# Optimization experiments

Measured on AMD Instinct MI355X. Metric: run time of the kernel, lower is better.

## Reference

```python
import jax, jax.numpy as jnp
import numpy as np

BERT_VOCAB_SIZE = 28996
INPUT_SIZE = 768
HIDDEN = 512
BI_H = 2 * HIDDEN


def _gru_cell(x, h, wih, whh, bih, bhh):
    # PyTorch GRUCell math. x: [I], h: [H]; wih: [3H, I], whh: [3H, H]
    H = h.shape[-1]
    gx = wih @ x + bih            # [3H]
    gh = whh @ h + bhh            # [3H]
    r = jax.nn.sigmoid(gx[:H] + gh[:H])
    z = jax.nn.sigmoid(gx[H:2 * H] + gh[H:2 * H])
    n = jnp.tanh(gx[2 * H:] + r * gh[2 * H:])
    return (1.0 - z) * n + z * h


def _run_gru(xs, h0, wih, whh, bih, bhh):
    def step(h, x):
        hn = _gru_cell(x, h, wih, whh, bih, bhh)
        return hn, hn
    _, hs = jax.lax.scan(step, h0, xs)
    return hs  # [L, H]


def setup_inputs() -> dict:
    key = jax.random.key(0)
    ks = jax.random.split(key, 16)
    s = 0.02
    inp = {
        'input_context': jax.random.normal(ks[0], (512, INPUT_SIZE), jnp.float32),
        'output_context': jax.random.normal(ks[1], (1024, INPUT_SIZE), jnp.float32),
        # forward encoder GRUCell
        'fw_wih': jax.random.normal(ks[2], (3 * HIDDEN, INPUT_SIZE), jnp.float32) * s,
        'fw_whh': jax.random.normal(ks[3], (3 * HIDDEN, HIDDEN), jnp.float32) * s,
        'fw_bih': jnp.zeros((3 * HIDDEN,), jnp.float32),
        'fw_bhh': jnp.zeros((3 * HIDDEN,), jnp.float32),
        # backward encoder GRUCell
        'bw_wih': jax.random.normal(ks[4], (3 * HIDDEN, INPUT_SIZE), jnp.float32) * s,
        'bw_whh': jax.random.normal(ks[5], (3 * HIDDEN, HIDDEN), jnp.float32) * s,
        'bw_bih': jnp.zeros((3 * HIDDEN,), jnp.float32),
        'bw_bhh': jnp.zeros((3 * HIDDEN,), jnp.float32),
        # decoder GRUCell (hidden = 2H)
        'dec_wih': jax.random.normal(ks[6], (3 * BI_H, INPUT_SIZE), jnp.float32) * s,
        'dec_whh': jax.random.normal(ks[7], (3 * BI_H, BI_H), jnp.float32) * s,
        'dec_bih': jnp.zeros((3 * BI_H,), jnp.float32),
        'dec_bhh': jnp.zeros((3 * BI_H,), jnp.float32),
        # vocab projection
        'W_pred': jax.random.normal(ks[8], (BI_H, BERT_VOCAB_SIZE), jnp.float32) * s,
    }
    return inp


def reference(input_context, output_context,
              fw_wih, fw_whh, fw_bih, fw_bhh,
              bw_wih, bw_whh, bw_bih, bw_bhh,
              dec_wih, dec_whh, dec_bih, dec_bhh,
              W_pred):
    h0 = jnp.zeros((HIDDEN,), input_context.dtype)
    # bidirectional encoder
    fwd_hs = _run_gru(input_context, h0, fw_wih, fw_whh, fw_bih, fw_bhh)        # [L, H]
    bwd_hs = _run_gru(input_context[::-1], h0, bw_wih, bw_whh, bw_bih, bw_bhh)[::-1]
    # column L-1 of cat((fwd, bwd), dim=0) -> [fwd_hs[-1]; bwd_hs[-1]]
    h_dec0 = jnp.concatenate([fwd_hs[-1], bwd_hs[-1]], axis=0)                   # [2H]
    # decoder inputs: step 0 uses output_context[0], step i>0 uses output_context[i-1]
    dec_in = jnp.concatenate([output_context[:1], output_context[:-1]], axis=0)  # [Lo, I]
    dec_hs = _run_gru(dec_in, h_dec0, dec_wih, dec_whh, dec_bih, dec_bhh)        # [Lo, 2H]
    preds = dec_hs @ W_pred                                                      # [Lo, V]
    return preds
```

## Files before the change

### kernel.cpp

```cpp
#include <hip/hip_runtime.h>
#include <math.h>


typedef unsigned long long u64;
typedef unsigned short ushort_t;
typedef __attribute__((ext_vector_type(8))) short short8;
typedef __attribute__((ext_vector_type(4))) float f32x4;

#define NV 28996
#define NRWG 64
#define NWORK 192
#define TRT 7264
#define VOCT 1816

__device__ __forceinline__ float sigmoidf_(float x) {
  return 1.0f / (1.0f + __expf(-x));
}
__device__ __forceinline__ float tanhf_(float x) {
  const float xx = fminf(fmaxf(x, -15.0f), 15.0f);
  const float e = __expf(2.0f * xx);
  return (e - 1.0f) / (e + 1.0f);
}
__device__ __forceinline__ ushort_t f2bf(float f) {
  union { float f; unsigned u; } c; c.f = f;
  unsigned u = c.u;
  u += 0x7fffu + ((u >> 16) & 1u);
  return (ushort_t)(u >> 16);
}

__device__ __forceinline__ u64 pack_ht(float h, unsigned tag) {
  union { float f; unsigned u; } c; c.f = h;
  return ((u64)tag << 32) | (u64)c.u;
}
__device__ __forceinline__ float pk_h(u64 v) {
  union { unsigned u; float f; } c; c.u = (unsigned)v; return c.f;
}
__device__ __forceinline__ void astore(u64* p, u64 v) {
  __hip_atomic_store(p, v, __ATOMIC_RELAXED, __HIP_MEMORY_SCOPE_AGENT);
}
__device__ __forceinline__ u64 aload(const u64* p) {
  return __hip_atomic_load((u64*)p, __ATOMIC_RELAXED, __HIP_MEMORY_SCOPE_AGENT);
}
__device__ __forceinline__ void astore32(unsigned* p, unsigned v) {
  __hip_atomic_store(p, v, __ATOMIC_RELAXED, __HIP_MEMORY_SCOPE_AGENT);
}
__device__ __forceinline__ unsigned aload32(const unsigned* p) {
  return __hip_atomic_load((unsigned*)p, __ATOMIC_RELAXED, __HIP_MEMORY_SCOPE_AGENT);
}
__device__ __forceinline__ void afadd32(unsigned* p, unsigned v) {
  __hip_atomic_fetch_add(p, v, __ATOMIC_RELAXED, __HIP_MEMORY_SCOPE_AGENT);
}
__device__ __forceinline__ u64 packf2(float a, float b) {
  union { float f; unsigned u; } ca, cb; ca.f = a; cb.f = b;
  return ((u64)cb.u << 32) | (u64)ca.u;
}

__global__ __launch_bounds__(512) void recur_fused(
    const float* __restrict__ input_context,
    const float* __restrict__ fw_wih,
    const float* __restrict__ fw_bih,
    const float* __restrict__ bw_wih,
    const float* __restrict__ bw_bih,
    const float* __restrict__ bhh_bw,
    const float* __restrict__ gxdec,
    const float* __restrict__ whh_fw,
    const float* __restrict__ bhh_fw,
    const float* __restrict__ whh_dec,
    const float* __restrict__ bhh_dec,
    u64* fwbuf,
    u64* decbuf,
    unsigned* progress,
    unsigned* gx_done,
    unsigned* tr_done,
    float* dec_hs,
    unsigned* dec_hs_b32,
    const float* __restrict__ output_context,
    const float* __restrict__ dec_wih,
    const float* __restrict__ dec_bih,
    const float* __restrict__ W_pred,
    ushort_t* Wt,
    float* __restrict__ outC,
    float* gxdec_w,
    int do_bf16, int gx_expected)
{
  __shared__ __align__(16) char SMEM[57344];
  const int tid = threadIdx.x;
  const int wg = blockIdx.x;
  const int wave = tid >> 6;
  const int lane = tid & 63;

  if (wg < NRWG) {
    float* Hs = (float*)SMEM;
    float* gxs = (float*)(SMEM + 8192);
    const int u0 = wg << 3;

    {
      const int r = (wave << 6) + lane;
      const float* inrow = input_context + (size_t)r * 768;
      const float* wbase = fw_wih + (size_t)u0 * 768;
      float acc[24];
#pragma unroll
      for (int c = 0; c < 24; ++c) acc[c] = 0.f;
      for (int k = 0; k < 768; k += 4) {
        const float4 in4 = *(const float4*)&inrow[k];
#pragma unroll
        for (int u8 = 0; u8 < 8; ++u8) {
#pragma unroll
          for (int g = 0; g < 3; ++g) {
            const float4 w4 =
                *(const float4*)&wbase[(size_t)(g * 512 + u8) * 768 + k];
            acc[u8 * 3 + g] +=
                w4.x * in4.x + w4.y * in4.y + w4.z * in4.z + w4.w * in4.w;
          }
        }
      }
#pragma unroll
      for (int u8 = 0; u8 < 8; ++u8)
#pragma unroll
        for (int g = 0; g < 3; ++g)
          gxs[r * 24 + u8 * 3 + g] =
              acc[u8 * 3 + g] + fw_bih[g * 512 + u0 + u8];
    }
    {
      const int u = u0 + wave;
      const float* in511 = input_context + (size_t)511 * 768;
      float b0 = 0.f, b1 = 0.f, b2 = 0.f;
      for (int k = lane; k < 768; k += 64) {
        const float x = in511[k];
        b0 += x * bw_wih[(size_t)u * 768 + k];
        b1 += x * bw_wih[(size_t)(512 + u) * 768 + k];
        b2 += x * bw_wih[(size_t)(1024 + u) * 768 + k];
      }
#pragma unroll
      for (int s = 1; s < 64; s <<= 1) {
        b0 += __shfl_xor(b0, s, 64);
        b1 += __shfl_xor(b1, s, 64);
        b2 += __shfl_xor(b2, s, 64);
      }
      if (lane == 0) {
        const float r = sigmoidf_(b0 + bw_bih[u] + bhh_bw[u]);
        const float z = sigmoidf_(b1 + bw_bih[512 + u] + bhh_bw[512 + u]);
        const float n =
            tanhf_(b2 + bw_bih[1024 + u] + r * bhh_bw[1024 + u]);
        astore(&decbuf[512 + u], pack_ht((1.0f - z) * n, 512u));
      }
    }
    __syncthreads();

    {
      const int u = u0 + wave;
      const float br = bhh_fw[u], bz = bhh_fw[512 + u], bn = bhh_fw[1024 + u];
      float4 wr[3][2];
#pragma unroll
      for (int g = 0; g < 3; ++g) {
        const float* w = whh_fw + (size_t)(g * 512 + u) * 512;
#pragma unroll
        for (int i = 0; i < 2; ++i)
          wr[g][i] = *(const float4*)&w[(i << 8) + (lane << 2)];
      }
      for (int t = 0; t < 512; ++t) {
        const u64* src = fwbuf + ((t & 1) << 9);
        float* hs = Hs + ((t & 1) << 9);
        if (wave == 0) {
          u64 v[8];
          for (;;) {
            bool ok = true;
#pragma unroll
            for (int j = 0; j < 8; ++j) {
              v[j] = aload(src + (j << 6) + lane);
              ok &= ((unsigned)(v[j] >> 32) >= (unsigned)t);
            }
            if (__all(ok)) break;
          }
#pragma unroll
          for (int j = 0; j < 8; ++j) hs[(j << 6) + lane] = pk_h(v[j]);
        }
        const float g0 = gxs[t * 24 + wave * 3 + 0];
        const float g1 = gxs[t * 24 + wave * 3 + 1];
        const float g2 = gxs[t * 24 + wave * 3 + 2];
        __syncthreads();
        const float4 ha = *(const float4*)&hs[lane << 2];
        const float4 hb = *(const float4*)&hs[256 + (lane << 2)];
        float p0 = wr[0][0].x * ha.x + wr[0][0].y * ha.y + wr[0][0].z * ha.z +
                   wr[0][0].w * ha.w + wr[0][1].x * hb.x + wr[0][1].y * hb.y +
                   wr[0][1].z * hb.z + wr[0][1].w * hb.w;
        float p1 = wr[1][0].x * ha.x + wr[1][0].y * ha.y + wr[1][0].z * ha.z +
                   wr[1][0].w * ha.w + wr[1][1].x * hb.x + wr[1][1].y * hb.y +
                   wr[1][1].z * hb.z + wr[1][1].w * hb.w;
        float p2 = wr[2][0].x * ha.x + wr[2][0].y * ha.y + wr[2][0].z * ha.z +
                   wr[2][0].w * ha.w + wr[2][1].x * hb.x + wr[2][1].y * hb.y +
                   wr[2][1].z * hb.z + wr[2][1].w * hb.w;
#pragma unroll
        for (int s = 1; s < 64; s <<= 1) {
          p0 += __shfl_xor(p0, s, 64);
          p1 += __shfl_xor(p1, s, 64);
          p2 += __shfl_xor(p2, s, 64);
        }
        if (lane == 0) {
          const float hold = hs[u];
          const float r = sigmoidf_(g0 + p0 + br);
          const float z = sigmoidf_(g1 + p1 + bz);
          const float n = tanhf_(g2 + r * (p2 + bn));
          const float hnew = (1.0f - z) * n + z * hold;
          if (t < 511)
            astore(fwbuf + (((t + 1) & 1) << 9) + u,
                   pack_ht(hnew, (unsigned)(t + 1)));
          else
            astore(decbuf + u, pack_ht(hnew, 512u));
        }
      }
    }
    __syncthreads();
    if (tid == 0 && gx_expected) {
      while (aload32(gx_done) < (unsigned)gx_expected)
        __builtin_amdgcn_s_sleep(8);
    }
    __syncthreads();

    {
      const int du0 = (wg << 4) + (wave << 1);
      float bb0[2], bb1[2], bb2[2];
      float4 wr[2][3][4];
#pragma unroll
      for (int uu = 0; uu < 2; ++uu) {
        bb0[uu] = bhh_dec[du0 + uu];
        bb1[uu] = bhh_dec[1024 + du0 + uu];
        bb2[uu] = bhh_dec[2048 + du0 + uu];
#pragma unroll
        for (int g = 0; g < 3; ++g) {
          const float* w = whh_dec + (size_t)(g * 1024 + du0 + uu) * 1024;
#pragma unroll
          for (int i = 0; i < 4; ++i)
            wr[uu][g][i] = *(const float4*)&w[(i << 8) + (lane << 2)];
        }
      }
      for (int td = 0; td < 1024; ++td) {
        const int t = 512 + td;
        const u64* src = decbuf + ((t & 1) << 10);
        float* hs = (float*)SMEM + ((t & 1) << 10);
        if (wave == 0) {
          u64 v[16];
          for (;;) {
            bool ok = true;
#pragma unroll
            for (int j = 0; j < 16; ++j) {
              v[j] = aload(src + (j << 6) + lane);
              ok &= ((unsigned)(v[j] >> 32) >= (unsigned)t);
            }
            if (__all(ok)) break;
          }
#pragma unroll
          for (int j = 0; j < 16; ++j) hs[(j << 6) + lane] = pk_h(v[j]);
        }
        const float* gx = gxdec + (size_t)td * 3072;
        float ga[2], gb[2], gc[2];
#pragma unroll
        for (int uu = 0; uu < 2; ++uu) {
          ga[uu] = gx[du0 + uu];
          gb[uu] = gx[1024 + du0 + uu];
          gc[uu] = gx[2048 + du0 + uu];
        }
        __syncthreads();
        if (wave == 7 && lane == 0 && td)
          astore32(progress + wg, (unsigned)td);
        float4 h4[4];
#pragma unroll
        for (int i = 0; i < 4; ++i)
          h4[i] = *(const float4*)&hs[(i << 8) + (lane << 2)];
        float hn0v = 0.f, hn1v = 0.f;
#pragma unroll
        for (int uu = 0; uu < 2; ++uu) {
          float p0 = 0.f, p1 = 0.f, p2 = 0.f;
#pragma unroll
          for (int i = 0; i < 4; ++i) {
            p0 += wr[uu][0][i].x * h4[i].x + wr[uu][0][i].y * h4[i].y +
                  wr[uu][0][i].z * h4[i].z + wr[uu][0][i].w * h4[i].w;
            p1 += wr[uu][1][i].x * h4[i].x + wr[uu][1][i].y * h4[i].y +
                  wr[uu][1][i].z * h4[i].z + wr[uu][1][i].w * h4[i].w;
            p2 += wr[uu][2][i].x * h4[i].x + wr[uu][2][i].y * h4[i].y +
                  wr[uu][2][i].z * h4[i].z + wr[uu][2][i].w * h4[i].w;
          }
#pragma unroll
          for (int s = 1; s < 64; s <<= 1) {
            p0 += __shfl_xor(p0, s, 64);
            p1 += __shfl_xor(p1, s, 64);
            p2 += __shfl_xor(p2, s, 64);
          }
          if (lane == 0) {
            const int u = du0 + uu;
            const float hold = hs[u];
            const float r = sigmoidf_(ga[uu] + p0 + bb0[uu]);
            const float z = sigmoidf_(gb[uu] + p1 + bb1[uu]);
            const float n = tanhf_(gc[uu] + r * (p2 + bb2[uu]));
            const float hnew = (1.0f - z) * n + z * hold;
            astore(decbuf + (((t + 1) & 1) << 10) + u,
                   pack_ht(hnew, (unsigned)(t + 1)));
            if (uu == 0) hn0v = hnew; else hn1v = hnew;
          }
        }
        if (lane == 0) {
          if (do_bf16) {
            const unsigned pk =
                (unsigned)f2bf(hn0v) | ((unsigned)f2bf(hn1v) << 16);
            astore32(&dec_hs_b32[(size_t)td * 512 + (du0 >> 1)], pk);
          } else {
            dec_hs[(size_t)td * 1024 + du0] = hn0v;
            dec_hs[(size_t)td * 1024 + du0 + 1] = hn1v;
          }
        }
      }
      __syncthreads();
      if (wave == 7 && lane == 0) astore32(progress + wg, 1024u);
    }
    return;
  }

  if (!do_bf16) return;
  const int wid = wg - NRWG;

  {
    float (*As)[132] = (float(*)[132])SMEM;
    float (*Bs)[132] = (float(*)[132])(SMEM + 16 * 132 * 4);
    const int cb = wid % 24, rb = wid / 24;
    const int n0 = cb * 128, m0 = rb * 128;
    float acc[8][8];
    if (tid < 256) {
#pragma unroll
      for (int i = 0; i < 8; ++i)
#pragma unroll
        for (int j = 0; j < 8; ++j) acc[i][j] = 0.f;
    }
    const int fl = tid >> 1, fk = (tid & 1) << 3;
    const int am = m0 + fl;
    const int asrow = (am == 0) ? 0 : am - 1;
    for (int k0 = 0; k0 < 768; k0 += 16) {
      if (tid < 256) {
        {
          const float* p = output_context + (size_t)asrow * 768 + k0 + fk;
          const float4 v0 = *(const float4*)p;
          const float4 v1 = *(const float4*)(p + 4);
          As[fk + 0][fl] = v0.x; As[fk + 1][fl] = v0.y;
          As[fk + 2][fl] = v0.z; As[fk + 3][fl] = v0.w;
          As[fk + 4][fl] = v1.x; As[fk + 5][fl] = v1.y;
          As[fk + 6][fl] = v1.z; As[fk + 7][fl] = v1.w;
        }
        {
          const float* p = dec_wih + (size_t)(n0 + fl) * 768 + k0 + fk;
          const float4 v0 = *(const float4*)p;
          const float4 v1 = *(const float4*)(p + 4);
          Bs[fk + 0][fl] = v0.x; Bs[fk + 1][fl] = v0.y;
          Bs[fk + 2][fl] = v0.z; Bs[fk + 3][fl] = v0.w;
          Bs[fk + 4][fl] = v1.x; Bs[fk + 5][fl] = v1.y;
          Bs[fk + 6][fl] = v1.z; Bs[fk + 7][fl] = v1.w;
        }
      }
      __syncthreads();
      if (tid < 256) {
        const int tx = tid & 15, ty = tid >> 4;
#pragma unroll
        for (int k = 0; k < 16; ++k) {
          const float4 a0 = *(const float4*)&As[k][ty << 3];
          const float4 a1 = *(const float4*)&As[k][(ty << 3) + 4];
          const float4 b0 = *(const float4*)&Bs[k][tx << 3];
          const float4 b1 = *(const float4*)&Bs[k][(tx << 3) + 4];
          const float av[8] = {a0.x, a0.y, a0.z, a0.w, a1.x, a1.y, a1.z, a1.w};
          const float bv[8] = {b0.x, b0.y, b0.z, b0.w, b1.x, b1.y, b1.z, b1.w};
#pragma unroll
          for (int i = 0; i < 8; ++i)
#pragma unroll
            for (int j = 0; j < 8; ++j) acc[i][j] += av[i] * bv[j];
        }
      }
      __syncthreads();
    }
    if (tid < 256) {
      const int tx = tid & 15, ty = tid >> 4;
      const int mb = m0 + (ty << 3), nb = n0 + (tx << 3);
#pragma unroll
      for (int i = 0; i < 8; ++i) {
        const int m = mb + i;
#pragma unroll
        for (int j = 0; j < 8; j += 2) {
          const float oa = acc[i][j] + dec_bih[nb + j];
          const float ob = acc[i][j + 1] + dec_bih[nb + j + 1];
          astore((u64*)&gxdec_w[(size_t)m * 3072 + nb + j], packf2(oa, ob));
        }
      }
    }
    __syncthreads();
    if (tid == 0) afadd32(gx_done, 1u);
  }

  {
    float (*T)[65] = (float(*)[65])SMEM;
    for (int i = wid; i < TRT; i += NWORK) {
      const int n0 = (i % 454) * 64;
      const int k0 = (i / 454) * 64;
      __syncthreads();
      if (tid < 256) {
        const int nloc = tid & 63, q = tid >> 6;
        const bool nok = (n0 + nloc) < NV;
#pragma unroll
        for (int r = 0; r < 16; ++r) {
          const int kloc = q + r * 4;
          T[kloc][nloc] =
              nok ? W_pred[(size_t)(k0 + kloc) * NV + n0 + nloc] : 0.f;
        }
      }
      __syncthreads();
      if (tid < 256) {
        const int nloc = tid >> 2;
        const int jb = (tid & 3) << 3;
        if (n0 + nloc < NV) {
          unsigned* dst =
              (unsigned*)Wt + (size_t)(n0 + nloc) * 512 + (k0 >> 1) + jb;
#pragma unroll
          for (int j = 0; j < 8; ++j) {
            const int kk = (jb + j) << 1;
            const unsigned pk = (unsigned)f2bf(T[kk][nloc]) |
                                ((unsigned)f2bf(T[kk + 1][nloc]) << 16);
            astore32(dst + j, pk);
          }
        }
      }
    }
    __syncthreads();
    if (tid == 0) afadd32(tr_done, 1u);
  }

  {
    if (wave == 0) {
      if (lane == 0)
        while (aload32(tr_done) < (unsigned)NWORK) __builtin_amdgcn_s_sleep(64);
    }
    __syncthreads();
    short* As = (short*)SMEM;
    short* Bs = As + 128 * 72;
    const ushort_t* A = (const ushort_t*)dec_hs_b32;
    const int wm = (tid >> 6) >> 1, wn = (tid >> 6) & 1;
    for (int i = wid; i < VOCT; i += NWORK) {
      const int rb = i / 227, cb = i % 227;
      const unsigned tgt = (unsigned)(rb * 128 + 128);
      if (wave == 0) {
        for (;;) {
          const unsigned p = aload32(progress + lane);
          if (__all(p >= tgt)) break;
          __builtin_amdgcn_s_sleep(64);
        }
      }
      __syncthreads();
      const int n0 = cb * 128, m0 = rb * 128;
      const int frow = tid >> 2;
      const int fko = (tid & 3) << 4;
      const bool bok = (n0 + frow) < NV;
      f32x4 acc[2][4];
#pragma unroll
      for (int a = 0; a < 2; ++a)
#pragma unroll
        for (int b = 0; b < 4; ++b) acc[a][b] = (f32x4){0.f, 0.f, 0.f, 0.f};
      for (int k0 = 0; k0 < 1024; k0 += 64) {
        {
          const uint4* s =
              (const uint4*)(A + (size_t)(m0 + frow) * 1024 + k0 + fko);
          uint4* d = (uint4*)&As[frow * 72 + fko];
          d[0] = s[0]; d[1] = s[1];
        }
        {
          uint4 v0 = make_uint4(0, 0, 0, 0), v1 = v0;
          if (bok) {
            const uint4* s =
                (const uint4*)(Wt + (size_t)(n0 + frow) * 1024 + k0 + fko);
            v0 = s[0]; v1 = s[1];
          }
          uint4* d = (uint4*)&Bs[frow * 72 + fko];
          d[0] = v0; d[1] = v1;
        }
        __syncthreads();
#pragma unroll
        for (int ks = 0; ks < 64; ks += 32) {
          short8 a[2], b[4];
#pragma unroll
          for (int fm = 0; fm < 2; ++fm)
            a[fm] = *(const short8*)&As[(wm * 32 + fm * 16 + (lane & 15)) * 72 +
                                        ks + ((lane >> 4) << 3)];
#pragma unroll
          for (int fn = 0; fn < 4; ++fn)
            b[fn] = *(const short8*)&Bs[(wn * 64 + fn * 16 + (lane & 15)) * 72 +
                                        ks + ((lane >> 4) << 3)];
#pragma unroll
          for (int fm = 0; fm < 2; ++fm)
#pragma unroll
            for (int fn = 0; fn < 4; ++fn)
              acc[fm][fn] = __builtin_amdgcn_mfma_f32_16x16x32_bf16(
                  a[fm], b[fn], acc[fm][fn], 0, 0, 0);
        }
        __syncthreads();
      }
#pragma unroll
      for (int fm = 0; fm < 2; ++fm) {
#pragma unroll
        for (int fn = 0; fn < 4; ++fn) {
          const int col = n0 + wn * 64 + fn * 16 + (lane & 15);
          if (col < NV) {
            const int rbase = m0 + wm * 32 + fm * 16 + ((lane >> 4) << 2);
#pragma unroll
            for (int r = 0; r < 4; ++r)
              outC[(size_t)(rbase + r) * NV + col] = acc[fm][fn][r];
          }
        }
      }
    }
  }
}

#define GBK 16
#define GLDS 132

template <int BT>
__global__ __launch_bounds__(256) void gemm128(
    const float* __restrict__ A, const float* __restrict__ B,
    const float* __restrict__ bias, float* __restrict__ C, int M, int N, int K,
    int rowmode, int fixedrow) {
  __shared__ float As[GBK][GLDS];
  __shared__ float Bs[GBK][GLDS];
  const int tid = threadIdx.x;
  const int n0 = blockIdx.x * 128;
  const int m0 = blockIdx.y * 128;
  const int tx = tid & 15;
  const int ty = tid >> 4;
  float acc[8][8];
#pragma unroll
  for (int i = 0; i < 8; ++i)
#pragma unroll
    for (int j = 0; j < 8; ++j) acc[i][j] = 0.f;

  const int fl = tid >> 1;
  const int fk = (tid & 1) << 3;
  const int am = m0 + fl;
  int asrow = am;
  if (rowmode == 1) asrow = (am == 0) ? 0 : am - 1;
  else if (rowmode == 2) asrow = fixedrow;
  const bool aok = (am < M);
  const bool nfull = (n0 + 128 <= N);

  for (int k0 = 0; k0 < K; k0 += GBK) {
    {
      float4 v0 = make_float4(0.f, 0.f, 0.f, 0.f), v1 = v0;
      if (aok) {
        const float* p = A + (size_t)asrow * K + k0 + fk;
        v0 = *(const float4*)p;
        v1 = *(const float4*)(p + 4);
      }
      As[fk + 0][fl] = v0.x; As[fk + 1][fl] = v0.y;
      As[fk + 2][fl] = v0.z; As[fk + 3][fl] = v0.w;
      As[fk + 4][fl] = v1.x; As[fk + 5][fl] = v1.y;
      As[fk + 6][fl] = v1.z; As[fk + 7][fl] = v1.w;
    }
    if (BT) {
      const int bn = n0 + fl;
      float4 v0 = make_float4(0.f, 0.f, 0.f, 0.f), v1 = v0;
      if (bn < N) {
        const float* p = B + (size_t)bn * K + k0 + fk;
        v0 = *(const float4*)p;
        v1 = *(const float4*)(p + 4);
      }
      Bs[fk + 0][fl] = v0.x; Bs[fk + 1][fl] = v0.y;
      Bs[fk + 2][fl] = v0.z; Bs[fk + 3][fl] = v0.w;
      Bs[fk + 4][fl] = v1.x; Bs[fk + 5][fl] = v1.y;
      Bs[fk + 6][fl] = v1.z; Bs[fk + 7][fl] = v1.w;
    } else {
      const int kl = tid >> 4;
      const int nq = (tid & 15) << 3;
      const float* p = B + (size_t)(k0 + kl) * N + n0 + nq;
      if (nfull) {
        *(float4*)&Bs[kl][nq] = *(const float4*)p;
        *(float4*)&Bs[kl][nq + 4] = *(const float4*)(p + 4);
      } else {
#pragma unroll
        for (int j = 0; j < 8; ++j)
          Bs[kl][nq + j] = (n0 + nq + j < N) ? p[j] : 0.f;
      }
    }
    __syncthreads();
#pragma unroll
    for (int k = 0; k < GBK; ++k) {
      const float4 a0 = *(const float4*)&As[k][ty << 3];
      const float4 a1 = *(const float4*)&As[k][(ty << 3) + 4];
      const float4 b0 = *(const float4*)&Bs[k][tx << 3];
      const float4 b1 = *(const float4*)&Bs[k][(tx << 3) + 4];
      const float av[8] = {a0.x, a0.y, a0.z, a0.w, a1.x, a1.y, a1.z, a1.w};
      const float bv[8] = {b0.x, b0.y, b0.z, b0.w, b1.x, b1.y, b1.z, b1.w};
#pragma unroll
      for (int i = 0; i < 8; ++i)
#pragma unroll
        for (int j = 0; j < 8; ++j) acc[i][j] += av[i] * bv[j];
    }
    __syncthreads();
  }

  const int mb = m0 + (ty << 3);
  const int nb = n0 + (tx << 3);
#pragma unroll
  for (int i = 0; i < 8; ++i) {
    const int m = mb + i;
    if (m >= M) continue;
    float o[8];
#pragma unroll
    for (int j = 0; j < 8; ++j) o[j] = acc[i][j];
    if (nfull) {
      if (bias) {
#pragma unroll
        for (int j = 0; j < 8; ++j) o[j] += bias[nb + j];
      }
      *(float4*)&C[(size_t)m * N + nb] = make_float4(o[0], o[1], o[2], o[3]);
      *(float4*)&C[(size_t)m * N + nb + 4] = make_float4(o[4], o[5], o[6], o[7]);
    } else {
#pragma unroll
      for (int j = 0; j < 8; ++j) {
        const int n = nb + j;
        if (n < N) C[(size_t)m * N + n] = o[j] + (bias ? bias[n] : 0.f);
      }
    }
  }
}

extern "C" void kernel_launch(void* const* d_in, const int* in_sizes, int n_in,
                              void* d_out, int out_size, void* d_ws,
                              size_t ws_size, hipStream_t stream) {
  (void)in_sizes; (void)n_in; (void)out_size;
  const float* input_context  = (const float*)d_in[0];
  const float* output_context = (const float*)d_in[1];
  const float* fw_wih = (const float*)d_in[2];
  const float* fw_whh = (const float*)d_in[3];
  const float* fw_bih = (const float*)d_in[4];
  const float* fw_bhh = (const float*)d_in[5];
  const float* bw_wih = (const float*)d_in[6];
  const float* bw_bih = (const float*)d_in[8];
  const float* bw_bhh = (const float*)d_in[9];
  const float* dec_wih = (const float*)d_in[10];
  const float* dec_whh = (const float*)d_in[11];
  const float* dec_bih = (const float*)d_in[12];
  const float* dec_bhh = (const float*)d_in[13];
  const float* W_pred  = (const float*)d_in[14];
  float* out = (float*)d_out;

  char* wsb = (char*)d_ws;
  u64* fwbuf   = (u64*)wsb;
  u64* decbuf  = (u64*)(wsb + 8192);
  unsigned* progress = (unsigned*)(wsb + 24576);
  unsigned* gx_done  = (unsigned*)(wsb + 24576 + 256);
  unsigned* tr_done  = (unsigned*)(wsb + 24576 + 260);
  float* gxdec = (float*)(wsb + 3176960);
  float* dec_hs = (float*)(wsb + 15759872);
  unsigned* dec_hs_b32 = (unsigned*)(wsb + 15759872);
  ushort_t* Wt = (ushort_t*)(wsb + 19954176);
  const int do_bf16 = (ws_size >= 79337984u) ? 1 : 0;

  hipMemsetAsync(d_ws, 0, 25088, stream);

  if (!do_bf16)
    gemm128<1><<<dim3(24, 8), dim3(256), 0, stream>>>(
        output_context, dec_wih, dec_bih, gxdec, 1024, 3072, 768, 1, 0);

  const int grid = do_bf16 ? (NRWG + NWORK) : NRWG;
  recur_fused<<<dim3(grid), dim3(512), 0, stream>>>(
      input_context, fw_wih, fw_bih, bw_wih, bw_bih, bw_bhh,
      gxdec, fw_whh, fw_bhh, dec_whh, dec_bhh,
      fwbuf, decbuf, progress, gx_done, tr_done, dec_hs, dec_hs_b32,
      output_context, dec_wih, dec_bih, W_pred, Wt, out, gxdec,
      do_bf16, do_bf16 ? NWORK : 0);

  if (!do_bf16)
    gemm128<0><<<dim3(227, 8), dim3(256), 0, stream>>>(
        dec_hs, W_pred, nullptr, out, 1024, NV, 1024, 0, 0);
}
```

Before: 4.980 ms.

## Pipeline hidden-state polling and merge decoder unit reductions across lanes

Replaces the spin-poll loops on the hidden-state exchange buffers with a triple-buffered poll that keeps three sets of atomic loads in flight. In the decoder, two waves now split the 1024-element poll between them. The per-wave pair of hidden units is computed with six interleaved butterfly reductions, and lanes 0 and 1 do the gate math in parallel instead of one lane doing it serially. The aim is to cut per-step latency on the sequential recurrence's critical path, at the cost of more registers and extra polling traffic.

```diff
diff --git a/kernel.cpp b/kernel.cpp
--- a/kernel.cpp
+++ b/kernel.cpp
@@ -53,6 +53,36 @@
 __device__ __forceinline__ u64 packf2(float a, float b) {
   union { float f; unsigned u; } ca, cb; ca.f = a; cb.f = b;
   return ((u64)cb.u << 32) | (u64)ca.u;
+}
+
+__device__ __forceinline__ void poll_load8(const u64* src, int lane, u64* b) {
+#pragma unroll
+  for (int j = 0; j < 8; ++j) b[j] = aload(src + (j << 6) + lane);
+}
+__device__ __forceinline__ bool poll_ok8(const u64* b, unsigned t) {
+  bool ok = true;
+#pragma unroll
+  for (int j = 0; j < 8; ++j) ok &= ((unsigned)(b[j] >> 32) >= t);
+  return __all(ok);
+}
+__device__ __forceinline__ void stage8(float* hs, int lane, const u64* b) {
+#pragma unroll
+  for (int j = 0; j < 8; ++j) hs[(j << 6) + lane] = pk_h(b[j]);
+}
+__device__ __forceinline__ void poll_pipelined(const u64* src, int lane,
+                                               unsigned t, float* hs) {
+  u64 b0[8], b1[8], b2[8];
+  poll_load8(src, lane, b0);
+  poll_load8(src, lane, b1);
+  poll_load8(src, lane, b2);
+  for (;;) {
+    if (poll_ok8(b0, t)) { stage8(hs, lane, b0); break; }
+    poll_load8(src, lane, b0);
+    if (poll_ok8(b1, t)) { stage8(hs, lane, b1); break; }
+    poll_load8(src, lane, b1);
+    if (poll_ok8(b2, t)) { stage8(hs, lane, b2); break; }
+    poll_load8(src, lane, b2);
+  }
 }
 
 __global__ __launch_bounds__(512) void recur_fused(
@@ -161,20 +191,8 @@
       for (int t = 0; t < 512; ++t) {
         const u64* src = fwbuf + ((t & 1) << 9);
         float* hs = Hs + ((t & 1) << 9);
-        if (wave == 0) {
-          u64 v[8];
-          for (;;) {
-            bool ok = true;
-#pragma unroll
-            for (int j = 0; j < 8; ++j) {
-              v[j] = aload(src + (j << 6) + lane);
-              ok &= ((unsigned)(v[j] >> 32) >= (unsigned)t);
-            }
-            if (__all(ok)) break;
-          }
-#pragma unroll
-          for (int j = 0; j < 8; ++j) hs[(j << 6) + lane] = pk_h(v[j]);
-        }
+        if (wave == 0)
+          poll_pipelined(src, lane, (unsigned)t, hs);
         const float g0 = gxs[t * 24 + wave * 3 + 0];
         const float g1 = gxs[t * 24 + wave * 3 + 1];
         const float g2 = gxs[t * 24 + wave * 3 + 2];
@@ -219,13 +237,12 @@
 
     {
       const int du0 = (wg << 4) + (wave << 1);
-      float bb0[2], bb1[2], bb2[2];
+      const float bbr0 = bhh_dec[du0], bbr1 = bhh_dec[du0 + 1];
+      const float bbz0 = bhh_dec[1024 + du0], bbz1 = bhh_dec[1024 + du0 + 1];
+      const float bbn0 = bhh_dec[2048 + du0], bbn1 = bhh_dec[2048 + du0 + 1];
       float4 wr[2][3][4];
 #pragma unroll
-      for (int uu = 0; uu < 2; ++uu) {
-        bb0[uu] = bhh_dec[du0 + uu];
-        bb1[uu] = bhh_dec[1024 + du0 + uu];
-        bb2[uu] = bhh_dec[2048 + du0 + uu];
+      for (int uu = 0; uu < 2; ++uu)
 #pragma unroll
         for (int g = 0; g < 3; ++g) {
           const float* w = whh_dec + (size_t)(g * 1024 + du0 + uu) * 1024;
@@ -233,33 +250,17 @@
           for (int i = 0; i < 4; ++i)
             wr[uu][g][i] = *(const float4*)&w[(i << 8) + (lane << 2)];
         }
-      }
       for (int td = 0; td < 1024; ++td) {
         const int t = 512 + td;
         const u64* src = decbuf + ((t & 1) << 10);
         float* hs = (float*)SMEM + ((t & 1) << 10);
-        if (wave == 0) {
-          u64 v[16];
-          for (;;) {
-            bool ok = true;
-#pragma unroll
-            for (int j = 0; j < 16; ++j) {
-              v[j] = aload(src + (j << 6) + lane);
-              ok &= ((unsigned)(v[j] >> 32) >= (unsigned)t);
-            }
-            if (__all(ok)) break;
-          }
-#pragma unroll
-          for (int j = 0; j < 16; ++j) hs[(j << 6) + lane] = pk_h(v[j]);
-        }
+        if (wave < 2)
+          poll_pipelined(src + (wave << 9), lane, (unsigned)t,
+                         hs + (wave << 9));
         const float* gx = gxdec + (size_t)td * 3072;
-        float ga[2], gb[2], gc[2];
-#pragma unroll
-        for (int uu = 0; uu < 2; ++uu) {
-          ga[uu] = gx[du0 + uu];
-          gb[uu] = gx[1024 + du0 + uu];
-          gc[uu] = gx[2048 + du0 + uu];
-        }
+        const float g_r0 = gx[du0], g_r1 = gx[du0 + 1];
+        const float g_z0 = gx[1024 + du0], g_z1 = gx[1024 + du0 + 1];
+        const float g_n0 = gx[2048 + du0], g_n1 = gx[2048 + du0 + 1];
         __syncthreads();
         if (wave == 7 && lane == 0 && td)
           astore32(progress + wg, (unsigned)td);
@@ -267,45 +268,59 @@
 #pragma unroll
         for (int i = 0; i < 4; ++i)
           h4[i] = *(const float4*)&hs[(i << 8) + (lane << 2)];
-        float hn0v = 0.f, hn1v = 0.f;
-#pragma unroll
-        for (int uu = 0; uu < 2; ++uu) {
-          float p0 = 0.f, p1 = 0.f, p2 = 0.f;
-#pragma unroll
-          for (int i = 0; i < 4; ++i) {
-            p0 += wr[uu][0][i].x * h4[i].x + wr[uu][0][i].y * h4[i].y +
-                  wr[uu][0][i].z * h4[i].z + wr[uu][0][i].w * h4[i].w;
-            p1 += wr[uu][1][i].x * h4[i].x + wr[uu][1][i].y * h4[i].y +
-                  wr[uu][1][i].z * h4[i].z + wr[uu][1][i].w * h4[i].w;
-            p2 += wr[uu][2][i].x * h4[i].x + wr[uu][2][i].y * h4[i].y +
-                  wr[uu][2][i].z * h4[i].z + wr[uu][2][i].w * h4[i].w;
-          }
-#pragma unroll
-          for (int s = 1; s < 64; s <<= 1) {
-            p0 += __shfl_xor(p0, s, 64);
-            p1 += __shfl_xor(p1, s, 64);
-            p2 += __shfl_xor(p2, s, 64);
-          }
-          if (lane == 0) {
-            const int u = du0 + uu;
-            const float hold = hs[u];
-            const float r = sigmoidf_(ga[uu] + p0 + bb0[uu]);
-            const float z = sigmoidf_(gb[uu] + p1 + bb1[uu]);
-            const float n = tanhf_(gc[uu] + r * (p2 + bb2[uu]));
-            const float hnew = (1.0f - z) * n + z * hold;
-            astore(decbuf + (((t + 1) & 1) << 10) + u,
-                   pack_ht(hnew, (unsigned)(t + 1)));
-            if (uu == 0) hn0v = hnew; else hn1v = hnew;
-          }
-        }
+        float pa0 = 0.f, pa1 = 0.f, pa2 = 0.f;
+        float pb0 = 0.f, pb1 = 0.f, pb2 = 0.f;
+#pragma unroll
+        for (int i = 0; i < 4; ++i) {
+          const float4 h = h4[i];
+          pa0 += wr[0][0][i].x * h.x + wr[0][0][i].y * h.y +
+                 wr[0][0][i].z * h.z + wr[0][0][i].w * h.w;
+          pa1 += wr[0][1][i].x * h.x + wr[0][1][i].y * h.y +
+                 wr[0][1][i].z * h.z + wr[0][1][i].w * h.w;
+          pa2 += wr[0][2][i].x * h.x + wr[0][2][i].y * h.y +
+                 wr[0][2][i].z * h.z + wr[0][2][i].w * h.w;
+          pb0 += wr[1][0][i].x * h.x + wr[1][0][i].y * h.y +
+                 wr[1][0][i].z * h.z + wr[1][0][i].w * h.w;
+          pb1 += wr[1][1][i].x * h.x + wr[1][1][i].y * h.y +
+                 wr[1][1][i].z * h.z + wr[1][1][i].w * h.w;
+          pb2 += wr[1][2][i].x * h.x + wr[1][2][i].y * h.y +
+                 wr[1][2][i].z * h.z + wr[1][2][i].w * h.w;
+        }
+#pragma unroll
+        for (int s = 1; s < 64; s <<= 1) {
+          pa0 += __shfl_xor(pa0, s, 64);
+          pa1 += __shfl_xor(pa1, s, 64);
+          pa2 += __shfl_xor(pa2, s, 64);
+          pb0 += __shfl_xor(pb0, s, 64);
+          pb1 += __shfl_xor(pb1, s, 64);
+          pb2 += __shfl_xor(pb2, s, 64);
+        }
+        const float S0 = lane ? pb0 : pa0;
+        const float S1 = lane ? pb1 : pa1;
+        const float S2 = lane ? pb2 : pa2;
+        const float G0 = lane ? g_r1 : g_r0;
+        const float G1 = lane ? g_z1 : g_z0;
+        const float G2 = lane ? g_n1 : g_n0;
+        const float B0 = lane ? bbr1 : bbr0;
+        const float B1 = lane ? bbz1 : bbz0;
+        const float B2 = lane ? bbn1 : bbn0;
+        const float hold = hs[du0 + (lane & 1)];
+        const float r = sigmoidf_(G0 + S0 + B0);
+        const float z = sigmoidf_(G1 + S1 + B1);
+        const float n = tanhf_(G2 + r * (S2 + B2));
+        const float hnew = (1.0f - z) * n + z * hold;
+        if (lane < 2)
+          astore(decbuf + (((t + 1) & 1) << 10) + du0 + lane,
+                 pack_ht(hnew, (unsigned)(t + 1)));
+        const float hn1 = __shfl(hnew, 1, 64);
         if (lane == 0) {
           if (do_bf16) {
             const unsigned pk =
-                (unsigned)f2bf(hn0v) | ((unsigned)f2bf(hn1v) << 16);
+                (unsigned)f2bf(hnew) | ((unsigned)f2bf(hn1) << 16);
             astore32(&dec_hs_b32[(size_t)td * 512 + (du0 >> 1)], pk);
           } else {
-            dec_hs[(size_t)td * 1024 + du0] = hn0v;
-            dec_hs[(size_t)td * 1024 + du0 + 1] = hn1v;
+            dec_hs[(size_t)td * 1024 + du0] = hnew;
+            dec_hs[(size_t)td * 1024 + du0 + 1] = hn1;
           }
         }
       }
```

Measured after the change: 6.141 ms. 1.23x slower.
